# Performance work log

Measured on AMD Instinct MI355X. Metric: run time of the kernel, lower is better.

The kernel has to match this reference:

```python
import jax, jax.numpy as jnp
import numpy as np

T, B = 1024, 16384
GAMMA = 0.99
LAMBDA = 0.97


def setup_inputs() -> dict:
    key = jax.random.key(0)
    k1, k2 = jax.random.split(key)
    value = jax.random.normal(k1, (T + 1, B), dtype=jnp.float32)
    reward = jax.random.normal(k2, (T, B), dtype=jnp.float32)
    return {"value": value, "reward": reward}


def reference(value, reward):
    # delta[t] = r[t] + gamma * V[t+1] - V[t]          shape (T, B)
    delta = reward + GAMMA * value[1:] - value[:-1]
    coef = jnp.float32(GAMMA * LAMBDA)

    def step(carry, d):
        adv_t = d + coef * carry
        return adv_t, adv_t

    init = jnp.zeros(delta.shape[1:], dtype=delta.dtype)
    # reverse-in-time scan: adv[t] = delta[t] + gamma*lambda * adv[t+1]
    _, adv = jax.lax.scan(step, init, delta, reverse=True)
    return adv
```

## Files before the change

kernel.cpp:

```cpp
#include <hip/hip_runtime.h>


constexpr int T = 1024;
constexpr int B = 16384;
constexpr int L = 32;
constexpr int C = T / L;
constexpr float GAMMA = (float)0.99;
constexpr float COEF  = (float)(0.99 * 0.97);

__host__ __device__ constexpr float pow_coef(int n) {
    float p = 1.0f;
    for (int i = 0; i < n; ++i) p *= COEF;
    return p;
}
constexpr float CL = pow_coef(L);

__global__ __launch_bounds__(256) void gae_chunk_scan(
    const float* __restrict__ value,
    const float* __restrict__ reward,
    float* __restrict__ S)
{
    const int c4    = blockIdx.x * blockDim.x + threadIdx.x;
    const int chunk = blockIdx.y;
    const int b     = c4 * 4;
    const int t0 = chunk * L;
    const int t1 = t0 + L;

    float4 vnext = *(const float4*)(value + (size_t)t1 * B + b);
    float4 s = make_float4(0.f, 0.f, 0.f, 0.f);

    #pragma unroll 4
    for (int t = t1 - 1; t >= t0; --t) {
        float4 r = *(const float4*)(reward + (size_t)t * B + b);
        float4 v = *(const float4*)(value  + (size_t)t * B + b);
        float dx = r.x + GAMMA * vnext.x - v.x;
        float dy = r.y + GAMMA * vnext.y - v.y;
        float dz = r.z + GAMMA * vnext.z - v.z;
        float dw = r.w + GAMMA * vnext.w - v.w;
        s.x = dx + COEF * s.x;
        s.y = dy + COEF * s.y;
        s.z = dz + COEF * s.z;
        s.w = dw + COEF * s.w;
        vnext = v;
    }
    *(float4*)(S + (size_t)chunk * B + b) = s;
}

__global__ __launch_bounds__(256) void gae_emit(
    const float* __restrict__ value,
    const float* __restrict__ reward,
    const float* __restrict__ S,
    float* __restrict__ out)
{
    const int c4    = blockIdx.x * blockDim.x + threadIdx.x;
    const int chunk = blockIdx.y;
    const int b     = c4 * 4;
    const int t0 = chunk * L;
    const int t1 = t0 + L;

    float4 carry = make_float4(0.f, 0.f, 0.f, 0.f);
    for (int j = C - 1; j > chunk; --j) {
        float4 sj = *(const float4*)(S + (size_t)j * B + b);
        carry.x = sj.x + CL * carry.x;
        carry.y = sj.y + CL * carry.y;
        carry.z = sj.z + CL * carry.z;
        carry.w = sj.w + CL * carry.w;
    }

    float4 adv = carry;
    float4 vnext = *(const float4*)(value + (size_t)t1 * B + b);

    #pragma unroll 4
    for (int t = t1 - 1; t >= t0; --t) {
        float4 r = *(const float4*)(reward + (size_t)t * B + b);
        float4 v = *(const float4*)(value  + (size_t)t * B + b);
        float dx = r.x + GAMMA * vnext.x - v.x;
        float dy = r.y + GAMMA * vnext.y - v.y;
        float dz = r.z + GAMMA * vnext.z - v.z;
        float dw = r.w + GAMMA * vnext.w - v.w;
        adv.x = dx + COEF * adv.x;
        adv.y = dy + COEF * adv.y;
        adv.z = dz + COEF * adv.z;
        adv.w = dw + COEF * adv.w;
        *(float4*)(out + (size_t)t * B + b) = adv;
        vnext = v;
    }
}

extern "C" void kernel_launch(void* const* d_in, const int* in_sizes, int n_in,
                              void* d_out, int out_size, void* d_ws, size_t ws_size,
                              hipStream_t stream) {
    const float* value  = (const float*)d_in[0];
    const float* reward = (const float*)d_in[1];
    float* out = (float*)d_out;
    float* S   = (float*)d_ws;

    dim3 block(256);
    dim3 grid(B / 4 / 256, C);

    gae_chunk_scan<<<grid, block, 0, stream>>>(value, reward, S);
    gae_emit<<<grid, block, 0, stream>>>(value, reward, S, out);
}
```

Baseline: 190.8 us.

## Fuse chunk scan and emit into cooperative kernel with grid sync

```diff
diff --git a/kernel.cpp b/kernel.cpp
--- a/kernel.cpp
+++ b/kernel.cpp
@@ -1,11 +1,14 @@
 #include <hip/hip_runtime.h>
+#include <hip/hip_cooperative_groups.h>
+
+namespace cg = cooperative_groups;
 
 
-constexpr int T = 1024;
-constexpr int B = 16384;
-constexpr int L = 32;
-constexpr int C = T / L;
-constexpr float GAMMA = (float)0.99;
+constexpr int T_ = 1024;
+constexpr int B_ = 16384;
+constexpr int L_ = 16;
+constexpr int C_ = T_ / L_;
+constexpr float GAMMA = 0.99f;
 constexpr float COEF  = (float)(0.99 * 0.97);
 
 __host__ __device__ constexpr float pow_coef(int n) {
@@ -13,7 +16,58 @@
     for (int i = 0; i < n; ++i) p *= COEF;
     return p;
 }
-constexpr float CL = pow_coef(L);
+constexpr float CL = pow_coef(L_);
+
+__device__ __forceinline__ float4 fmaf4(float4 a, float c, float4 b) {
+    return make_float4(a.x + c * b.x, a.y + c * b.y, a.z + c * b.z, a.w + c * b.w);
+}
+
+__global__ __launch_bounds__(256, 4) void gae_fused(
+    const float* __restrict__ value,
+    const float* __restrict__ reward,
+    float* __restrict__ S,
+    float* __restrict__ out)
+{
+    const int c4    = blockIdx.x * blockDim.x + threadIdx.x;
+    const int chunk = blockIdx.y;
+    const size_t b  = (size_t)c4 * 4;
+    const int t0    = chunk * L_;
+
+    float4 d[L_];
+    float4 vnext = *(const float4*)(value + (size_t)(t0 + L_) * B_ + b);
+    #pragma unroll
+    for (int i = L_ - 1; i >= 0; --i) {
+        const int t = t0 + i;
+        float4 r = *(const float4*)(reward + (size_t)t * B_ + b);
+        float4 v = *(const float4*)(value  + (size_t)t * B_ + b);
+        d[i].x = r.x + GAMMA * vnext.x - v.x;
+        d[i].y = r.y + GAMMA * vnext.y - v.y;
+        d[i].z = r.z + GAMMA * vnext.z - v.z;
+        d[i].w = r.w + GAMMA * vnext.w - v.w;
+        vnext = v;
+    }
+
+    float4 s = make_float4(0.f, 0.f, 0.f, 0.f);
+    #pragma unroll
+    for (int i = L_ - 1; i >= 0; --i) s = fmaf4(d[i], COEF, s);
+    *(float4*)(S + (size_t)chunk * B_ + b) = s;
+
+    cg::this_grid().sync();
+
+    float4 carry = make_float4(0.f, 0.f, 0.f, 0.f);
+    #pragma unroll 4
+    for (int j = C_ - 1; j > chunk; --j) {
+        float4 sj = *(const float4*)(S + (size_t)j * B_ + b);
+        carry = fmaf4(sj, CL, carry);
+    }
+
+    float4 a = carry;
+    #pragma unroll
+    for (int i = L_ - 1; i >= 0; --i) {
+        a = fmaf4(d[i], COEF, a);
+        *(float4*)(out + (size_t)(t0 + i) * B_ + b) = a;
+    }
+}
 
 __global__ __launch_bounds__(256) void gae_chunk_scan(
     const float* __restrict__ value,
@@ -22,28 +76,24 @@
 {
     const int c4    = blockIdx.x * blockDim.x + threadIdx.x;
     const int chunk = blockIdx.y;
-    const int b     = c4 * 4;
-    const int t0 = chunk * L;
-    const int t1 = t0 + L;
+    const size_t b  = (size_t)c4 * 4;
+    const int t0 = chunk * L_;
 
-    float4 vnext = *(const float4*)(value + (size_t)t1 * B + b);
+    float4 vnext = *(const float4*)(value + (size_t)(t0 + L_) * B_ + b);
     float4 s = make_float4(0.f, 0.f, 0.f, 0.f);
-
-    #pragma unroll 4
-    for (int t = t1 - 1; t >= t0; --t) {
-        float4 r = *(const float4*)(reward + (size_t)t * B + b);
-        float4 v = *(const float4*)(value  + (size_t)t * B + b);
-        float dx = r.x + GAMMA * vnext.x - v.x;
-        float dy = r.y + GAMMA * vnext.y - v.y;
-        float dz = r.z + GAMMA * vnext.z - v.z;
-        float dw = r.w + GAMMA * vnext.w - v.w;
-        s.x = dx + COEF * s.x;
-        s.y = dy + COEF * s.y;
-        s.z = dz + COEF * s.z;
-        s.w = dw + COEF * s.w;
+    #pragma unroll
+    for (int t = t0 + L_ - 1; t >= t0; --t) {
+        float4 r = *(const float4*)(reward + (size_t)t * B_ + b);
+        float4 v = *(const float4*)(value  + (size_t)t * B_ + b);
+        float4 dd;
+        dd.x = r.x + GAMMA * vnext.x - v.x;
+        dd.y = r.y + GAMMA * vnext.y - v.y;
+        dd.z = r.z + GAMMA * vnext.z - v.z;
+        dd.w = r.w + GAMMA * vnext.w - v.w;
+        s = fmaf4(dd, COEF, s);
         vnext = v;
     }
-    *(float4*)(S + (size_t)chunk * B + b) = s;
+    *(float4*)(S + (size_t)chunk * B_ + b) = s;
 }
 
 __global__ __launch_bounds__(256) void gae_emit(
@@ -54,35 +104,29 @@
 {
     const int c4    = blockIdx.x * blockDim.x + threadIdx.x;
     const int chunk = blockIdx.y;
-    const int b     = c4 * 4;
-    const int t0 = chunk * L;
-    const int t1 = t0 + L;
+    const size_t b  = (size_t)c4 * 4;
+    const int t0 = chunk * L_;
 
     float4 carry = make_float4(0.f, 0.f, 0.f, 0.f);
-    for (int j = C - 1; j > chunk; --j) {
-        float4 sj = *(const float4*)(S + (size_t)j * B + b);
-        carry.x = sj.x + CL * carry.x;
-        carry.y = sj.y + CL * carry.y;
-        carry.z = sj.z + CL * carry.z;
-        carry.w = sj.w + CL * carry.w;
+    #pragma unroll 4
+    for (int j = C_ - 1; j > chunk; --j) {
+        float4 sj = *(const float4*)(S + (size_t)j * B_ + b);
+        carry = fmaf4(sj, CL, carry);
     }
 
-    float4 adv = carry;
-    float4 vnext = *(const float4*)(value + (size_t)t1 * B + b);
-
-    #pragma unroll 4
-    for (int t = t1 - 1; t >= t0; --t) {
-        float4 r = *(const float4*)(reward + (size_t)t * B + b);
-        float4 v = *(const float4*)(value  + (size_t)t * B + b);
-        float dx = r.x + GAMMA * vnext.x - v.x;
-        float dy = r.y + GAMMA * vnext.y - v.y;
-        float dz = r.z + GAMMA * vnext.z - v.z;
-        float dw = r.w + GAMMA * vnext.w - v.w;
-        adv.x = dx + COEF * adv.x;
-        adv.y = dy + COEF * adv.y;
-        adv.z = dz + COEF * adv.z;
-        adv.w = dw + COEF * adv.w;
-        *(float4*)(out + (size_t)t * B + b) = adv;
+    float4 a = carry;
+    float4 vnext = *(const float4*)(value + (size_t)(t0 + L_) * B_ + b);
+    #pragma unroll
+    for (int t = t0 + L_ - 1; t >= t0; --t) {
+        float4 r = *(const float4*)(reward + (size_t)t * B_ + b);
+        float4 v = *(const float4*)(value  + (size_t)t * B_ + b);
+        float4 dd;
+        dd.x = r.x + GAMMA * vnext.x - v.x;
+        dd.y = r.y + GAMMA * vnext.y - v.y;
+        dd.z = r.z + GAMMA * vnext.z - v.z;
+        dd.w = r.w + GAMMA * vnext.w - v.w;
+        a = fmaf4(dd, COEF, a);
+        *(float4*)(out + (size_t)t * B_ + b) = a;
         vnext = v;
     }
 }
@@ -96,8 +140,13 @@
     float* S   = (float*)d_ws;
 
     dim3 block(256);
-    dim3 grid(B / 4 / 256, C);
+    dim3 grid(B_ / 4 / 256, C_);
 
-    gae_chunk_scan<<<grid, block, 0, stream>>>(value, reward, S);
-    gae_emit<<<grid, block, 0, stream>>>(value, reward, S, out);
+    void* args[] = {(void*)&value, (void*)&reward, (void*)&S, (void*)&out};
+    hipError_t err = hipLaunchCooperativeKernel((void*)gae_fused, grid, block,
+                                                args, 0, stream);
+    if (err != hipSuccess) {
+        gae_chunk_scan<<<grid, block, 0, stream>>>(value, reward, S);
+        gae_emit<<<grid, block, 0, stream>>>(value, reward, S, out);
+    }
 }
```

Result: slower. 297.6 us (+56.0%).
